# Kernel optimization log

Measured on AMD Instinct MI355X. Metric: run time of the kernel, lower is better.

The kernel has to match this reference:

```python
import jax, jax.numpy as jnp
import numpy as np

B, S, D, H = 4, 2048, 1024, 16
HD = D // H  # head_size = 64


def setup_inputs() -> dict:
    key = jax.random.key(0)
    ks = jax.random.split(key, 9)
    sc = 0.02
    x = jax.random.normal(ks[0], (B, S, D), dtype=jnp.float32)
    Wq = jax.random.normal(ks[1], (H, D, HD), dtype=jnp.float32) * sc
    Wk = jax.random.normal(ks[2], (H, D, HD), dtype=jnp.float32) * sc
    Wv = jax.random.normal(ks[3], (H, D, HD), dtype=jnp.float32) * sc
    bq = jax.random.normal(ks[4], (H, HD), dtype=jnp.float32) * sc
    bk = jax.random.normal(ks[5], (H, HD), dtype=jnp.float32) * sc
    bv = jax.random.normal(ks[6], (H, HD), dtype=jnp.float32) * sc
    Wp = jax.random.normal(ks[7], (D, D), dtype=jnp.float32) * sc
    bp = jax.random.normal(ks[8], (D,), dtype=jnp.float32) * sc
    return {"x": x, "Wq": Wq, "bq": bq, "Wk": Wk, "bk": bk,
            "Wv": Wv, "bv": bv, "Wp": Wp, "bp": bp}


def reference(x, Wq, bq, Wk, bk, Wv, bv, Wp, bp):
    # Per-head Linear q/k/v, batched over heads with einsum (equivalent math
    # to the original Python loop over SingleHeadAttention modules).
    q = jnp.einsum('bsd,hde->bhse', x, Wq) + bq[None, :, None, :]
    k = jnp.einsum('bsd,hde->bhse', x, Wk) + bk[None, :, None, :]
    v = jnp.einsum('bsd,hde->bhse', x, Wv) + bv[None, :, None, :]
    att = jnp.einsum('bhqe,bhke->bhqk', q, k) / jnp.sqrt(jnp.asarray(HD, q.dtype))
    causal = jnp.tril(jnp.ones((S, S), dtype=bool))  # [S,S]
    att = jnp.where(causal[None, None], att, jnp.finfo(att.dtype).min)
    w = jax.nn.softmax(att, axis=-1)
    o = jnp.einsum('bhqk,bhke->bhqe', w, v)           # [B,H,S,HD]
    o = o.transpose(0, 2, 1, 3).reshape(B, S, D)      # concat heads on last dim
    # output projection; dropout is identity in eval (p=0.0)
    return jnp.einsum('bsd,de->bse', o, Wp) + bp
```

## Files before the change

### kernel.cpp

```cpp
#include <hip/hip_runtime.h>
#include <hip/hip_bf16.h>

typedef __attribute__((ext_vector_type(8)))  short bf16x8;
typedef __attribute__((ext_vector_type(4)))  float f32x4;
typedef __attribute__((ext_vector_type(16))) float f32x16;
typedef __attribute__((ext_vector_type(2)))  int   i32x2;

#define NH  16
#define HD  64
#define SEQ 2048
#define DM  1024
#define NB  4

#define QSCALE 0.18033688011112042f

#define MFMA(a,b,c)   __builtin_amdgcn_mfma_f32_16x16x32_bf16((a),(b),(c),0,0,0)
#define MFMA32(a,b,c) __builtin_amdgcn_mfma_f32_32x32x16_bf16((a),(b),(c),0,0,0)

static __device__ __forceinline__ void gload_lds16(const void* g, void* l) {
    __builtin_amdgcn_global_load_lds(
        (const __attribute__((address_space(1))) void*)g,
        (__attribute__((address_space(3))) void*)l, 16, 0, 0);
}

__global__ __launch_bounds__(256)
void prep(const float* __restrict__ x,  const float* __restrict__ Wq,
          const float* __restrict__ Wk, const float* __restrict__ Wv,
          const float* __restrict__ Wp,
          __hip_bfloat16* __restrict__ xb,  __hip_bfloat16* __restrict__ wqt,
          __hip_bfloat16* __restrict__ wkt, __hip_bfloat16* __restrict__ wvt,
          __hip_bfloat16* __restrict__ wpt) {
    const long XE = (long)NB * SEQ * DM;
    const long CAST_T = XE / 8;
    long gid = (long)blockIdx.x * 256 + threadIdx.x;
    if (gid < CAST_T) {
        long i = gid * 8;
        float4 a = *reinterpret_cast<const float4*>(x + i);
        float4 b = *reinterpret_cast<const float4*>(x + i + 4);
        ushort4 o1, o2;
        o1.x = __bfloat16_as_ushort(__float2bfloat16(a.x));
        o1.y = __bfloat16_as_ushort(__float2bfloat16(a.y));
        o1.z = __bfloat16_as_ushort(__float2bfloat16(a.z));
        o1.w = __bfloat16_as_ushort(__float2bfloat16(a.w));
        o2.x = __bfloat16_as_ushort(__float2bfloat16(b.x));
        o2.y = __bfloat16_as_ushort(__float2bfloat16(b.y));
        o2.z = __bfloat16_as_ushort(__float2bfloat16(b.z));
        o2.w = __bfloat16_as_ushort(__float2bfloat16(b.w));
        *reinterpret_cast<ushort4*>(xb + i)     = o1;
        *reinterpret_cast<ushort4*>(xb + i + 4) = o2;
        return;
    }
    long r = gid - CAST_T;
    const long WQK = 1 << 20;
    if (r < 3 * WQK) {
        int z = (int)(r >> 20);
        long idx = r & (WQK - 1);
        const float* src = (z == 0) ? Wq : (z == 1) ? Wk : Wv;
        __hip_bfloat16* dst = (z == 0) ? wqt : (z == 1) ? wkt : wvt;
        int c  = (int)(idx & 63);
        long t2 = idx >> 6;
        int rr = (int)(t2 & 1023);
        int mm = (int)(t2 >> 10);
        dst[((long)mm * HD + c) * DM + rr] = __float2bfloat16(src[idx]);
    } else {
        long idx = r - 3 * WQK;
        int c  = (int)(idx & 1023);
        int rr = (int)(idx >> 10);
        wpt[(long)c * DM + rr] = __float2bfloat16(Wp[idx]);
    }
}

__global__ __launch_bounds__(256)
void qkv_gemm(const __hip_bfloat16* __restrict__ A,
              const __hip_bfloat16* __restrict__ BT,
              const float* __restrict__ b0,
              const float* __restrict__ b1,
              const float* __restrict__ b2,
              __hip_bfloat16* __restrict__ Qo,
              __hip_bfloat16* __restrict__ Ko,
              __hip_bfloat16* __restrict__ Vto) {
    __shared__ __align__(16) char lds[2][32768];
    int tid = threadIdx.x;
    int w = tid >> 6, l = tid & 63;
    int lr = l & 15, lg = l >> 4;
    int wr = w >> 1, wc = w & 1;
    int mtile = blockIdx.x, ntile = blockIdx.y;
    const int AR0 = mtile * 128, BR0 = ntile * 128;

    const int rsub = w * 8 + (l >> 3);
    const int sg0 = l & 7;
    auto stage = [&](const __hip_bfloat16* g, int grow0, int kc, char* lbase) {
#pragma unroll
        for (int i = 0; i < 4; ++i) {
            int row = i * 32 + rsub;
            gload_lds16(g + (long)(grow0 + row) * DM + kc + ((sg0 ^ (row & 7)) << 3),
                        lbase + i * 4096 + w * 1024);
        }
    };

    int aoff[4][2], boff[4][2];
#pragma unroll
    for (int m = 0; m < 4; ++m) {
        int ra = wr * 64 + m * 16 + lr;
        int rb = wc * 64 + m * 16 + lr;
#pragma unroll
        for (int kh = 0; kh < 2; ++kh) {
            aoff[m][kh] = ra * 128 + (((kh * 4 + lg) ^ (ra & 7)) << 4);
            boff[m][kh] = 16384 + rb * 128 + (((kh * 4 + lg) ^ (rb & 7)) << 4);
        }
    }

    f32x4 acc[4][4] = {};

    stage(A,  AR0, 0, lds[0]);
    stage(BT, BR0, 0, lds[0] + 16384);
    __syncthreads();

    int cur = 0;
    for (int kt = 0; kt < 16; ++kt) {
        if (kt < 15) {
            int kc = (kt + 1) * 64;
            stage(A,  AR0, kc, lds[cur ^ 1]);
            stage(BT, BR0, kc, lds[cur ^ 1] + 16384);
        }
        bf16x8 bf[4][2];
#pragma unroll
        for (int n = 0; n < 4; ++n) {
            bf[n][0] = *(const bf16x8*)(lds[cur] + boff[n][0]);
            bf[n][1] = *(const bf16x8*)(lds[cur] + boff[n][1]);
        }
#pragma unroll
        for (int m = 0; m < 4; ++m) {
            bf16x8 a0 = *(const bf16x8*)(lds[cur] + aoff[m][0]);
            bf16x8 a1 = *(const bf16x8*)(lds[cur] + aoff[m][1]);
#pragma unroll
            for (int n = 0; n < 4; ++n) {
                acc[m][n] = MFMA(a0, bf[n][0], acc[m][n]);
                acc[m][n] = MFMA(a1, bf[n][1], acc[m][n]);
            }
        }
        __syncthreads();
        cur ^= 1;
    }

    int z = ntile >> 3;
    const float* bias = (z == 0) ? b0 : (z == 1) ? b1 : b2;
    int colbase = (ntile & 7) * 128 + wc * 64;
#pragma unroll
    for (int n = 0; n < 4; ++n) {
        int hc = colbase + n * 16 + lr;
        int h = hc >> 6, e = hc & 63;
        float bb = bias[hc];
#pragma unroll
        for (int m = 0; m < 4; ++m) {
            int row0 = mtile * 128 + wr * 64 + m * 16 + lg * 4;
            int b = row0 >> 11, s0 = row0 & 2047;
            if (z == 0) {
#pragma unroll
                for (int r = 0; r < 4; ++r)
                    Qo[(((long)b * NH + h) * SEQ + s0 + r) * HD + e] =
                        __float2bfloat16((acc[m][n][r] + bb) * QSCALE);
            } else if (z == 1) {
#pragma unroll
                for (int r = 0; r < 4; ++r)
                    Ko[(((long)b * NH + h) * SEQ + s0 + r) * HD + e] =
                        __float2bfloat16(acc[m][n][r] + bb);
            } else {
                ushort4 s4;
                s4.x = __bfloat16_as_ushort(__float2bfloat16(acc[m][n][0] + bb));
                s4.y = __bfloat16_as_ushort(__float2bfloat16(acc[m][n][1] + bb));
                s4.z = __bfloat16_as_ushort(__float2bfloat16(acc[m][n][2] + bb));
                s4.w = __bfloat16_as_ushort(__float2bfloat16(acc[m][n][3] + bb));
                *reinterpret_cast<ushort4*>(
                    Vto + ((long)(b * NH + h) * HD + e) * SEQ + s0) = s4;
            }
        }
    }
}

__global__ __launch_bounds__(256)
void out_gemm(const __hip_bfloat16* __restrict__ A,
              const __hip_bfloat16* __restrict__ BT,
              const float* __restrict__ b0,
              float* __restrict__ Fo) {
    __shared__ __align__(16) char smem[2][16384];
    int tid = threadIdx.x;
    int w = tid >> 6, l = tid & 63;
    int wr = w >> 1, wc = w & 1;
    int lr = l & 15, lg = l >> 4;
    int mtile = blockIdx.x, ntile = blockIdx.y;

    const __hip_bfloat16* Ab = A  + (long)mtile * 128 * DM;
    const __hip_bfloat16* Bb = BT + (long)ntile * 128 * DM;

    const int srow0 = tid >> 2;
    const int srow1 = 64 + srow0;
    const int g0 = (tid & 3) ^ ((srow0 >> 1) & 3);

    int aoff[4], boff[4];
#pragma unroll
    for (int m = 0; m < 4; ++m) {
        int ra = wr * 64 + m * 16 + lr;
        aoff[m] = ra * 64 + ((lg ^ ((ra >> 1) & 3)) * 16);
        int rb = wc * 64 + m * 16 + lr;
        boff[m] = 8192 + rb * 64 + ((lg ^ ((rb >> 1) & 3)) * 16);
    }

    f32x4 acc[4][4] = {};

    {
        char* base = smem[0] + w * 1024;
        gload_lds16(Ab + (long)srow0 * DM + g0 * 8, base);
        gload_lds16(Ab + (long)srow1 * DM + g0 * 8, base + 4096);
        gload_lds16(Bb + (long)srow0 * DM + g0 * 8, base + 8192);
        gload_lds16(Bb + (long)srow1 * DM + g0 * 8, base + 12288);
    }
    __syncthreads();

    int cur = 0;
    for (int kt = 0; kt < 32; ++kt) {
        if (kt != 31) {
            int k0 = (kt + 1) * 32;
            char* base = smem[cur ^ 1] + w * 1024;
            gload_lds16(Ab + (long)srow0 * DM + k0 + g0 * 8, base);
            gload_lds16(Ab + (long)srow1 * DM + k0 + g0 * 8, base + 4096);
            gload_lds16(Bb + (long)srow0 * DM + k0 + g0 * 8, base + 8192);
            gload_lds16(Bb + (long)srow1 * DM + k0 + g0 * 8, base + 12288);
        }
        bf16x8 af[4], bf[4];
#pragma unroll
        for (int m = 0; m < 4; ++m)
            af[m] = *reinterpret_cast<const bf16x8*>(smem[cur] + aoff[m]);
#pragma unroll
        for (int n = 0; n < 4; ++n)
            bf[n] = *reinterpret_cast<const bf16x8*>(smem[cur] + boff[n]);
#pragma unroll
        for (int m = 0; m < 4; ++m)
#pragma unroll
            for (int n = 0; n < 4; ++n)
                acc[m][n] = MFMA(af[m], bf[n], acc[m][n]);
        __syncthreads();
        cur ^= 1;
    }

#pragma unroll
    for (int n = 0; n < 4; ++n) {
        int col = ntile * 128 + wc * 64 + n * 16 + lr;
        float bb = b0[col];
#pragma unroll
        for (int m = 0; m < 4; ++m) {
            long row0 = mtile * 128 + wr * 64 + m * 16 + lg * 4;
#pragma unroll
            for (int r = 0; r < 4; ++r)
                Fo[(row0 + r) * DM + col] = acc[m][n][r] + bb;
        }
    }
}

static __device__ __forceinline__ unsigned pkbf(float a, float b) {
    __hip_bfloat162 h = __float22bfloat162_rn(float2{a, b});
    union { __hip_bfloat162 h2; unsigned u; } u_; u_.h2 = h;
    return u_.u;
}
static __device__ __forceinline__ bf16x8 make_pb(unsigned w0, unsigned w1,
                                                 unsigned w2, unsigned w3) {
    union { unsigned u[4]; bf16x8 v; } u_;
    u_.u[0] = w0; u_.u[1] = w1; u_.u[2] = w2; u_.u[3] = w3;
    return u_.v;
}
static __device__ __forceinline__ i32x2 pl32swap(unsigned a, unsigned b) {
    return __builtin_amdgcn_permlane32_swap((int)a, (int)b, false, false);
}
static __device__ __forceinline__ float xmax32(float x) {
    i32x2 r = pl32swap(__float_as_uint(x), __float_as_uint(x));
    return fmaxf(__uint_as_float((unsigned)r[0]), __uint_as_float((unsigned)r[1]));
}
static __device__ __forceinline__ float xsum32(float x) {
    i32x2 r = pl32swap(__float_as_uint(x), __float_as_uint(x));
    return __uint_as_float((unsigned)r[0]) + __uint_as_float((unsigned)r[1]);
}

template<bool MASKED>
static __device__ __forceinline__ void attn_tile(
    const bf16x8* kf, const bf16x8* qf, const bf16x8* vf,
    int lo5, int hi,
    f32x16& o0, f32x16& o1, float& m, float& lsum) {
    f32x16 st = {};
    __builtin_amdgcn_s_setprio(1);
#pragma unroll
    for (int kd = 0; kd < 4; ++kd) st = MFMA32(kf[kd], qf[kd], st);
    __builtin_amdgcn_s_setprio(0);
    if (MASKED) {
#pragma unroll
        for (int r = 0; r < 16; ++r) {
            int kvloc = (r & 3) + 8 * (r >> 2) + 4 * hi;
            st[r] = (kvloc > lo5) ? -INFINITY : st[r];
        }
    }
    float t0 = fmaxf(st[0], st[1]),   t1 = fmaxf(st[2], st[3]);
    float t2 = fmaxf(st[4], st[5]),   t3 = fmaxf(st[6], st[7]);
    float t4 = fmaxf(st[8], st[9]),   t5 = fmaxf(st[10], st[11]);
    float t6 = fmaxf(st[12], st[13]), t7 = fmaxf(st[14], st[15]);
    t0 = fmaxf(t0, t1); t2 = fmaxf(t2, t3); t4 = fmaxf(t4, t5); t6 = fmaxf(t6, t7);
    float tm = xmax32(fmaxf(fmaxf(t0, t2), fmaxf(t4, t6)));
    if (!__all(tm <= m + 11.0f)) {
        float mnew = fmaxf(m, tm);
        float fac = __builtin_amdgcn_exp2f(m - mnew);
        lsum *= fac;
#pragma unroll
        for (int r = 0; r < 16; ++r) { o0[r] *= fac; o1[r] *= fac; }
        m = mnew;
    }
    float p[16];
#pragma unroll
    for (int r = 0; r < 16; ++r) p[r] = __builtin_amdgcn_exp2f(st[r] - m);
    float s0 = (p[0] + p[1]) + (p[2] + p[3]);
    float s1 = (p[4] + p[5]) + (p[6] + p[7]);
    float s2 = (p[8] + p[9]) + (p[10] + p[11]);
    float s3 = (p[12] + p[13]) + (p[14] + p[15]);
    lsum += xsum32((s0 + s1) + (s2 + s3));

    unsigned pk0 = pkbf(p[0],  p[1]),  pk1 = pkbf(p[2],  p[3]);
    unsigned pk2 = pkbf(p[4],  p[5]),  pk3 = pkbf(p[6],  p[7]);
    unsigned pk4 = pkbf(p[8],  p[9]),  pk5 = pkbf(p[10], p[11]);
    unsigned pk6 = pkbf(p[12], p[13]), pk7 = pkbf(p[14], p[15]);
    i32x2 s02 = pl32swap(pk0, pk2);
    i32x2 s13 = pl32swap(pk1, pk3);
    i32x2 s46 = pl32swap(pk4, pk6);
    i32x2 s57 = pl32swap(pk5, pk7);
    bf16x8 pb0 = make_pb((unsigned)s02[0], (unsigned)s13[0],
                         (unsigned)s02[1], (unsigned)s13[1]);
    bf16x8 pb1 = make_pb((unsigned)s46[0], (unsigned)s57[0],
                         (unsigned)s46[1], (unsigned)s57[1]);

    __builtin_amdgcn_s_setprio(1);
    o0 = MFMA32(vf[0], pb0, o0);
    o1 = MFMA32(vf[1], pb0, o1);
    o0 = MFMA32(vf[2], pb1, o0);
    o1 = MFMA32(vf[3], pb1, o1);
    __builtin_amdgcn_s_setprio(0);
}

__global__ __launch_bounds__(256)
void flash_attn(const __hip_bfloat16* __restrict__ Q,
                const __hip_bfloat16* __restrict__ K,
                const __hip_bfloat16* __restrict__ Vt,
                __hip_bfloat16* __restrict__ O) {
    int bh = blockIdx.x;
    int w  = threadIdx.x >> 6, l = threadIdx.x & 63;
    int lo5 = l & 31, hi = l >> 5;
    int pair = blockIdx.y * 4 + w;
    int jA = pair, jB = 63 - pair;
    int q0A = jA * 32, q0B = jB * 32;

    const __hip_bfloat16* Qh = Q  + (long)bh * SEQ * HD;
    const __hip_bfloat16* Kh = K  + (long)bh * SEQ * HD;
    const __hip_bfloat16* Vh = Vt + (long)bh * HD * SEQ;

    bf16x8 qfA[4], qfB[4];
#pragma unroll
    for (int kd = 0; kd < 4; ++kd) {
        qfA[kd] = *reinterpret_cast<const bf16x8*>(
            Qh + (long)(q0A + lo5) * HD + kd * 16 + hi * 8);
        qfB[kd] = *reinterpret_cast<const bf16x8*>(
            Qh + (long)(q0B + lo5) * HD + kd * 16 + hi * 8);
    }

    f32x16 oA0 = {}, oA1 = {}, oB0 = {}, oB1 = {};
    float mA = -INFINITY, lsA = 0.f, mB = -INFINITY, lsB = 0.f;

    bf16x8 k0[4], k1[4], v0[4], v1[4];

#define LOADK(T, DST)                                                      \
    _Pragma("unroll")                                                      \
    for (int kd = 0; kd < 4; ++kd)                                         \
        DST[kd] = *reinterpret_cast<const bf16x8*>(                        \
            Kh + (long)((T) * 32 + lo5) * HD + kd * 16 + hi * 8);

#define LOADV(T, DST)                                                      \
    DST[0] = *reinterpret_cast<const bf16x8*>(                             \
        Vh + (long)(lo5) * SEQ + (T) * 32 + hi * 8);                       \
    DST[1] = *reinterpret_cast<const bf16x8*>(                             \
        Vh + (long)(32 + lo5) * SEQ + (T) * 32 + hi * 8);                  \
    DST[2] = *reinterpret_cast<const bf16x8*>(                             \
        Vh + (long)(lo5) * SEQ + (T) * 32 + 16 + hi * 8);                  \
    DST[3] = *reinterpret_cast<const bf16x8*>(                             \
        Vh + (long)(32 + lo5) * SEQ + (T) * 32 + 16 + hi * 8);

#define TILE_B(KK, VV)  attn_tile<false>(KK, qfB, VV, lo5, hi, oB0, oB1, mB, lsB)
#define TILE_A(KK, VV)  attn_tile<false>(KK, qfA, VV, lo5, hi, oA0, oA1, mA, lsA)
#define DIAG_A(KK, VV)  attn_tile<true >(KK, qfA, VV, lo5, hi, oA0, oA1, mA, lsA)
#define DIAG_B(KK, VV)  attn_tile<true >(KK, qfB, VV, lo5, hi, oB0, oB1, mB, lsB)

#define PHASE2(KA_, VA_, KB_, VB_)                                         \
    {                                                                      \
        int u = jA + 1;                                                    \
        while (u + 1 < jB) {                                               \
            LOADK(u + 1, KB_); LOADV(u + 1, VB_);                          \
            TILE_B(KA_, VA_);                                              \
            LOADK(u + 2, KA_); LOADV(u + 2, VA_);                          \
            TILE_B(KB_, VB_);                                              \
            u += 2;                                                        \
        }                                                                  \
        if (u < jB) {                                                      \
            LOADK(jB, KB_); LOADV(jB, VB_);                                \
            TILE_B(KA_, VA_);                                              \
            DIAG_B(KB_, VB_);                                              \
        } else {                                                           \
            DIAG_B(KA_, VA_);                                              \
        }                                                                  \
    }

    LOADK(0, k0); LOADV(0, v0);

    int t = 0;
    while (t + 1 < jA) {
        LOADK(t + 1, k1); LOADV(t + 1, v1);
        TILE_B(k0, v0);
        TILE_A(k0, v0);
        LOADK(t + 2, k0); LOADV(t + 2, v0);
        TILE_B(k1, v1);
        TILE_A(k1, v1);
        t += 2;
    }
    if (t < jA) {
        LOADK(jA, k1); LOADV(jA, v1);
        TILE_B(k0, v0);
        TILE_A(k0, v0);
        LOADK(jA + 1, k0); LOADV(jA + 1, v0);
        DIAG_A(k1, v1);
        TILE_B(k1, v1);
        PHASE2(k0, v0, k1, v1)
    } else {
        LOADK(jA + 1, k1); LOADV(jA + 1, v1);
        DIAG_A(k0, v0);
        TILE_B(k0, v0);
        PHASE2(k1, v1, k0, v0)
    }

#undef LOADK
#undef LOADV
#undef TILE_B
#undef TILE_A
#undef DIAG_A
#undef DIAG_B
#undef PHASE2

    int b = bh >> 4, h = bh & 15;
#pragma unroll
    for (int c = 0; c < 2; ++c) {
        int q0 = c ? q0B : q0A;
        const f32x16& o0 = c ? oB0 : oA0;
        const f32x16& o1 = c ? oB1 : oA1;
        float inv = 1.0f / (c ? lsB : lsA);
        __hip_bfloat16* orow = O + ((long)b * SEQ + q0 + lo5) * DM + h * HD;
#pragma unroll
        for (int nd = 0; nd < 2; ++nd) {
#pragma unroll
            for (int rg = 0; rg < 4; ++rg) {
                ushort4 s4;
                float a0 = (nd ? o1[rg * 4 + 0] : o0[rg * 4 + 0]) * inv;
                float a1 = (nd ? o1[rg * 4 + 1] : o0[rg * 4 + 1]) * inv;
                float a2 = (nd ? o1[rg * 4 + 2] : o0[rg * 4 + 2]) * inv;
                float a3 = (nd ? o1[rg * 4 + 3] : o0[rg * 4 + 3]) * inv;
                s4.x = __bfloat16_as_ushort(__float2bfloat16(a0));
                s4.y = __bfloat16_as_ushort(__float2bfloat16(a1));
                s4.z = __bfloat16_as_ushort(__float2bfloat16(a2));
                s4.w = __bfloat16_as_ushort(__float2bfloat16(a3));
                *reinterpret_cast<ushort4*>(orow + nd * 32 + rg * 8 + hi * 4) = s4;
            }
        }
    }
}

extern "C" void kernel_launch(void* const* d_in, const int* in_sizes, int n_in,
                              void* d_out, int out_size, void* d_ws, size_t ws_size,
                              hipStream_t stream) {
    const float* x  = (const float*)d_in[0];
    const float* Wq = (const float*)d_in[1];
    const float* bq = (const float*)d_in[2];
    const float* Wk = (const float*)d_in[3];
    const float* bk = (const float*)d_in[4];
    const float* Wv = (const float*)d_in[5];
    const float* bv = (const float*)d_in[6];
    const float* Wp = (const float*)d_in[7];
    const float* bp = (const float*)d_in[8];
    float* out = (float*)d_out;

    char* ws = (char*)d_ws;
    const long XE = (long)NB * SEQ * DM;
    const long QKV_ELEMS = (long)NB * NH * SEQ * HD;
    __hip_bfloat16* xb   = (__hip_bfloat16*)ws; ws += XE * 2;
    __hip_bfloat16* Qws  = (__hip_bfloat16*)ws; ws += QKV_ELEMS * 2;
    __hip_bfloat16* Kws  = (__hip_bfloat16*)ws; ws += QKV_ELEMS * 2;
    __hip_bfloat16* Vtws = (__hip_bfloat16*)ws; ws += QKV_ELEMS * 2;
    __hip_bfloat16* Ows  = (__hip_bfloat16*)ws; ws += QKV_ELEMS * 2;
    __hip_bfloat16* wqt  = (__hip_bfloat16*)ws; ws += (long)NH * DM * HD * 2;
    __hip_bfloat16* wkt  = (__hip_bfloat16*)ws; ws += (long)NH * DM * HD * 2;
    __hip_bfloat16* wvt  = (__hip_bfloat16*)ws; ws += (long)NH * DM * HD * 2;
    __hip_bfloat16* wpt  = (__hip_bfloat16*)ws; ws += (long)DM * DM * 2;

    prep<<<20480, 256, 0, stream>>>(x, Wq, Wk, Wv, Wp, xb, wqt, wkt, wvt, wpt);

    qkv_gemm<<<dim3(64, 24), 256, 0, stream>>>(
        xb, wqt, bq, bk, bv, Qws, Kws, Vtws);

    flash_attn<<<dim3(64, 8), 256, 0, stream>>>(Qws, Kws, Vtws, Ows);

    out_gemm<<<dim3(64, 8), 256, 0, stream>>>(Ows, wpt, bp, out);
}
```

Baseline: 221.3 us.

## Split KV range across two waves per query pair and merge via LDS

Each query-pair is now handled by two waves that process alternating KV tiles (even/odd), doubling the flash-attention grid. Their partial outputs and softmax statistics are combined through shared memory with a log-sum-exp style merge before writing. This targets the serial KV loop latency and low occupancy, at the cost of dropping the explicit double-buffered register prefetch, adding an LDS reduction plus barrier, and using about 35 KB of shared memory per block. Launch bounds now request 3 blocks per SM.

New measurement: 240.7 us. 1.09x slower.

```diff
diff --git a/kernel.cpp b/kernel.cpp
--- a/kernel.cpp
+++ b/kernel.cpp
@@ -341,15 +341,17 @@
     __builtin_amdgcn_s_setprio(0);
 }
 
-__global__ __launch_bounds__(256)
+__global__ __launch_bounds__(256, 3)
 void flash_attn(const __hip_bfloat16* __restrict__ Q,
                 const __hip_bfloat16* __restrict__ K,
                 const __hip_bfloat16* __restrict__ Vt,
                 __hip_bfloat16* __restrict__ O) {
+    __shared__ float mbuf[2][68][64];
     int bh = blockIdx.x;
     int w  = threadIdx.x >> 6, l = threadIdx.x & 63;
     int lo5 = l & 31, hi = l >> 5;
-    int pair = blockIdx.y * 4 + w;
+    int pair = blockIdx.y * 2 + (w >> 1);
+    int hw = w & 1;
     int jA = pair, jB = 63 - pair;
     int q0A = jA * 32, q0B = jB * 32;
 
@@ -369,82 +371,69 @@
     f32x16 oA0 = {}, oA1 = {}, oB0 = {}, oB1 = {};
     float mA = -INFINITY, lsA = 0.f, mB = -INFINITY, lsB = 0.f;
 
-    bf16x8 k0[4], k1[4], v0[4], v1[4];
-
-#define LOADK(T, DST)                                                      \
+    bf16x8 kf[4], vf[4];
+
+#define LOADKV(T)                                                          \
     _Pragma("unroll")                                                      \
     for (int kd = 0; kd < 4; ++kd)                                         \
-        DST[kd] = *reinterpret_cast<const bf16x8*>(                        \
-            Kh + (long)((T) * 32 + lo5) * HD + kd * 16 + hi * 8);
-
-#define LOADV(T, DST)                                                      \
-    DST[0] = *reinterpret_cast<const bf16x8*>(                             \
+        kf[kd] = *reinterpret_cast<const bf16x8*>(                         \
+            Kh + (long)((T) * 32 + lo5) * HD + kd * 16 + hi * 8);          \
+    vf[0] = *reinterpret_cast<const bf16x8*>(                              \
         Vh + (long)(lo5) * SEQ + (T) * 32 + hi * 8);                       \
-    DST[1] = *reinterpret_cast<const bf16x8*>(                             \
+    vf[1] = *reinterpret_cast<const bf16x8*>(                              \
         Vh + (long)(32 + lo5) * SEQ + (T) * 32 + hi * 8);                  \
-    DST[2] = *reinterpret_cast<const bf16x8*>(                             \
+    vf[2] = *reinterpret_cast<const bf16x8*>(                              \
         Vh + (long)(lo5) * SEQ + (T) * 32 + 16 + hi * 8);                  \
-    DST[3] = *reinterpret_cast<const bf16x8*>(                             \
+    vf[3] = *reinterpret_cast<const bf16x8*>(                              \
         Vh + (long)(32 + lo5) * SEQ + (T) * 32 + 16 + hi * 8);
 
-#define TILE_B(KK, VV)  attn_tile<false>(KK, qfB, VV, lo5, hi, oB0, oB1, mB, lsB)
-#define TILE_A(KK, VV)  attn_tile<false>(KK, qfA, VV, lo5, hi, oA0, oA1, mA, lsA)
-#define DIAG_A(KK, VV)  attn_tile<true >(KK, qfA, VV, lo5, hi, oA0, oA1, mA, lsA)
-#define DIAG_B(KK, VV)  attn_tile<true >(KK, qfB, VV, lo5, hi, oB0, oB1, mB, lsB)
-
-#define PHASE2(KA_, VA_, KB_, VB_)                                         \
-    {                                                                      \
-        int u = jA + 1;                                                    \
-        while (u + 1 < jB) {                                               \
-            LOADK(u + 1, KB_); LOADV(u + 1, VB_);                          \
-            TILE_B(KA_, VA_);                                              \
-            LOADK(u + 2, KA_); LOADV(u + 2, VA_);                          \
-            TILE_B(KB_, VB_);                                              \
-            u += 2;                                                        \
-        }                                                                  \
-        if (u < jB) {                                                      \
-            LOADK(jB, KB_); LOADV(jB, VB_);                                \
-            TILE_B(KA_, VA_);                                              \
-            DIAG_B(KB_, VB_);                                              \
-        } else {                                                           \
-            DIAG_B(KA_, VA_);                                              \
-        }                                                                  \
-    }
-
-    LOADK(0, k0); LOADV(0, v0);
-
-    int t = 0;
-    while (t + 1 < jA) {
-        LOADK(t + 1, k1); LOADV(t + 1, v1);
-        TILE_B(k0, v0);
-        TILE_A(k0, v0);
-        LOADK(t + 2, k0); LOADV(t + 2, v0);
-        TILE_B(k1, v1);
-        TILE_A(k1, v1);
+    int t = hw;
+    for (; t < jA; t += 2) {
+        LOADKV(t);
+        attn_tile<false>(kf, qfB, vf, lo5, hi, oB0, oB1, mB, lsB);
+        attn_tile<false>(kf, qfA, vf, lo5, hi, oA0, oA1, mA, lsA);
+    }
+    if (t == jA) {
+        LOADKV(t);
+        attn_tile<true >(kf, qfA, vf, lo5, hi, oA0, oA1, mA, lsA);
+        attn_tile<false>(kf, qfB, vf, lo5, hi, oB0, oB1, mB, lsB);
         t += 2;
     }
-    if (t < jA) {
-        LOADK(jA, k1); LOADV(jA, v1);
-        TILE_B(k0, v0);
-        TILE_A(k0, v0);
-        LOADK(jA + 1, k0); LOADV(jA + 1, v0);
-        DIAG_A(k1, v1);
-        TILE_B(k1, v1);
-        PHASE2(k0, v0, k1, v1)
-    } else {
-        LOADK(jA + 1, k1); LOADV(jA + 1, v1);
-        DIAG_A(k0, v0);
-        TILE_B(k0, v0);
-        PHASE2(k1, v1, k0, v0)
-    }
-
-#undef LOADK
-#undef LOADV
-#undef TILE_B
-#undef TILE_A
-#undef DIAG_A
-#undef DIAG_B
-#undef PHASE2
+    for (; t < jB; t += 2) {
+        LOADKV(t);
+        attn_tile<false>(kf, qfB, vf, lo5, hi, oB0, oB1, mB, lsB);
+    }
+    if (t == jB) {
+        LOADKV(t);
+        attn_tile<true >(kf, qfB, vf, lo5, hi, oB0, oB1, mB, lsB);
+    }
+#undef LOADKV
+
+    int p = w >> 1;
+    if (hw == 1) {
+#pragma unroll
+        for (int r = 0; r < 16; ++r) {
+            mbuf[p][r][l]      = oA0[r];
+            mbuf[p][16 + r][l] = oA1[r];
+            mbuf[p][32 + r][l] = oB0[r];
+            mbuf[p][48 + r][l] = oB1[r];
+        }
+        mbuf[p][64][l] = mA; mbuf[p][65][l] = lsA;
+        mbuf[p][66][l] = mB; mbuf[p][67][l] = lsB;
+    }
+    __syncthreads();
+    if (hw == 1) return;
+
+    float m1A = mbuf[p][64][l], l1A = mbuf[p][65][l];
+    float m1B = mbuf[p][66][l], l1B = mbuf[p][67][l];
+    float mmA = fmaxf(mA, m1A);
+    float fA0 = __builtin_amdgcn_exp2f(mA  - mmA);
+    float fA1 = __builtin_amdgcn_exp2f(m1A - mmA);
+    float invA = 1.0f / (lsA * fA0 + l1A * fA1);
+    float mmB = fmaxf(mB, m1B);
+    float fB0 = __builtin_amdgcn_exp2f(mB  - mmB);
+    float fB1 = __builtin_amdgcn_exp2f(m1B - mmB);
+    float invB = 1.0f / (lsB * fB0 + l1B * fB1);
 
     int b = bh >> 4, h = bh & 15;
 #pragma unroll
@@ -452,17 +441,24 @@
         int q0 = c ? q0B : q0A;
         const f32x16& o0 = c ? oB0 : oA0;
         const f32x16& o1 = c ? oB1 : oA1;
-        float inv = 1.0f / (c ? lsB : lsA);
+        float f0  = c ? fB0 : fA0;
+        float f1  = c ? fB1 : fA1;
+        float inv = c ? invB : invA;
+        int base = c * 32;
         __hip_bfloat16* orow = O + ((long)b * SEQ + q0 + lo5) * DM + h * HD;
 #pragma unroll
         for (int nd = 0; nd < 2; ++nd) {
 #pragma unroll
             for (int rg = 0; rg < 4; ++rg) {
                 ushort4 s4;
-                float a0 = (nd ? o1[rg * 4 + 0] : o0[rg * 4 + 0]) * inv;
-                float a1 = (nd ? o1[rg * 4 + 1] : o0[rg * 4 + 1]) * inv;
-                float a2 = (nd ? o1[rg * 4 + 2] : o0[rg * 4 + 2]) * inv;
-                float a3 = (nd ? o1[rg * 4 + 3] : o0[rg * 4 + 3]) * inv;
+                float a0 = ((nd ? o1[rg*4+0] : o0[rg*4+0]) * f0 +
+                            mbuf[p][base + nd*16 + rg*4 + 0][l] * f1) * inv;
+                float a1 = ((nd ? o1[rg*4+1] : o0[rg*4+1]) * f0 +
+                            mbuf[p][base + nd*16 + rg*4 + 1][l] * f1) * inv;
+                float a2 = ((nd ? o1[rg*4+2] : o0[rg*4+2]) * f0 +
+                            mbuf[p][base + nd*16 + rg*4 + 2][l] * f1) * inv;
+                float a3 = ((nd ? o1[rg*4+3] : o0[rg*4+3]) * f0 +
+                            mbuf[p][base + nd*16 + rg*4 + 3][l] * f1) * inv;
                 s4.x = __bfloat16_as_ushort(__float2bfloat16(a0));
                 s4.y = __bfloat16_as_ushort(__float2bfloat16(a1));
                 s4.z = __bfloat16_as_ushort(__float2bfloat16(a2));
@@ -505,7 +501,7 @@
     qkv_gemm<<<dim3(64, 24), 256, 0, stream>>>(
         xb, wqt, bq, bk, bv, Qws, Kws, Vtws);
 
-    flash_attn<<<dim3(64, 8), 256, 0, stream>>>(Qws, Kws, Vtws, Ows);
+    flash_attn<<<dim3(64, 16), 256, 0, stream>>>(Qws, Kws, Vtws, Ows);
 
     out_gemm<<<dim3(64, 8), 256, 0, stream>>>(Ows, wpt, bp, out);
 }
```
